# Kernel optimization log

Hardware: AMD Instinct MI355X
Metric: run time of the kernel (lower is better)

The kernel has to match this reference:

```python
import jax, jax.numpy as jnp
import numpy as np

N = 50000      # nodes
E = 1600000    # edges
D = 64         # in_channels (== hidden so layers stack)
H = 64         # hidden_channels
L = 3          # num_layers
G = 128        # graphs in batch
OUT = 1        # out_channels
BN_EPS = 1e-5


def setup_inputs() -> dict:
    key = jax.random.key(0)
    ks = jax.random.split(key, 8)
    s = 0.1
    x = jax.random.normal(ks[0], (N, D), dtype=jnp.float32)
    edge_index = jax.random.randint(ks[1], (2, E), 0, N, dtype=jnp.int64)
    batch = jnp.sort(jax.random.randint(ks[2], (N,), 0, G, dtype=jnp.int64))
    # stacked GINConv MLP params: Linear(D,H) -> BN(H) -> ReLU -> Linear(H,H)
    W1 = jax.random.normal(ks[3], (L, D, H), dtype=jnp.float32) * s
    b1 = jnp.zeros((L, H), jnp.float32)
    gamma = jnp.ones((L, H), jnp.float32)
    beta = jnp.zeros((L, H), jnp.float32)
    W2 = jax.random.normal(ks[4], (L, H, H), dtype=jnp.float32) * s
    b2 = jnp.zeros((L, H), jnp.float32)
    # head MLP: Linear(H,H) -> ReLU -> (dropout, eval mode) -> Linear(H,OUT)
    Wh1 = jax.random.normal(ks[5], (H, H), dtype=jnp.float32) * s
    bh1 = jnp.zeros((H,), jnp.float32)
    Wh2 = jax.random.normal(ks[6], (H, OUT), dtype=jnp.float32) * s
    bh2 = jnp.zeros((OUT,), jnp.float32)
    return dict(x=x, edge_index=edge_index, batch=batch,
                W1=W1, b1=b1, gamma=gamma, beta=beta, W2=W2, b2=b2,
                Wh1=Wh1, bh1=bh1, Wh2=Wh2, bh2=bh2)


def reference(x, edge_index, batch, W1, b1, gamma, beta, W2, b2, Wh1, bh1, Wh2, bh2):
    src, dst = edge_index[0], edge_index[1]

    def gin_layer(h, p):
        w1, bb1, g, be, w2, bb2 = p
        # scatter-add neighbor aggregation: sum_{j->i} h_j
        agg = jax.ops.segment_sum(h[src], dst, num_segments=N)  # [N, H]
        z = (agg + h) @ w1 + bb1  # (1+eps)*x + agg, eps=0; then Linear
        # BatchNorm1d (training-mode batch stats, biased var)
        mu = z.mean(0)
        var = ((z - mu) ** 2).mean(0)
        z = (z - mu) * jax.lax.rsqrt(var + BN_EPS) * g + be
        z = jax.nn.relu(z) @ w2 + bb2  # ReLU -> Linear (plain last layer)
        return jax.nn.relu(z), None    # outer .relu() in GIN.forward

    h, _ = jax.lax.scan(gin_layer, x, (W1, b1, gamma, beta, W2, b2))

    # global_mean_pool over batch ids
    cnt = jax.ops.segment_sum(jnp.ones((N, 1), h.dtype), batch, num_segments=G)
    pooled = jax.ops.segment_sum(h, batch, num_segments=G) / jnp.maximum(cnt, 1.0)

    # head MLP (dropout = identity in eval mode)
    return jax.nn.relu(pooled @ Wh1 + bh1) @ Wh2 + bh2
```

## Files before the change

kernel.cpp:

```cpp
#include <hip/hip_runtime.h>

#define N_NODES 50000
#define N_EDGES 1600000
#define HDIM 64
#define NLAYERS 3
#define NGRAPH 128
#define BN_EPS 1e-5f
#define CAP 96
#define NBINS 196
#define NBLK 782

__device__ __forceinline__ unsigned short f2bf(float f) {
    union { float f; unsigned u; } v; v.f = f;
    unsigned r = v.u + 0x7fffu + ((v.u >> 16) & 1u);
    return (unsigned short)(r >> 16);
}
__device__ __forceinline__ unsigned pack2(float a, float b) {
    return (unsigned)f2bf(a) | ((unsigned)f2bf(b) << 16);
}
__device__ __forceinline__ float bf2f(unsigned short b) {
    union { unsigned u; float f; } v; v.u = ((unsigned)b) << 16; return v.f;
}
__device__ __forceinline__ void acc8(float* a, uint4 v) {
    union { unsigned u; float f; } t;
    t.u = v.x << 16;         a[0] += t.f;
    t.u = v.x & 0xffff0000u; a[1] += t.f;
    t.u = v.y << 16;         a[2] += t.f;
    t.u = v.y & 0xffff0000u; a[3] += t.f;
    t.u = v.z << 16;         a[4] += t.f;
    t.u = v.z & 0xffff0000u; a[5] += t.f;
    t.u = v.w << 16;         a[6] += t.f;
    t.u = v.w & 0xffff0000u; a[7] += t.f;
}

__global__ __launch_bounds__(256) void hist1_kernel(
    const int* __restrict__ dst, int* __restrict__ gh)
{
    __shared__ int lh[NBINS];
    int tid = threadIdx.x;
    for (int i = tid; i < NBINS; i += 256) lh[i] = 0;
    __syncthreads();
    int t8 = blockIdx.x * 256 + tid;
    if (t8 < N_EDGES / 8) {
        int4 d0 = ((const int4*)dst)[t8 * 2];
        int4 d1 = ((const int4*)dst)[t8 * 2 + 1];
        atomicAdd(&lh[d0.x >> 8], 1);
        atomicAdd(&lh[d0.y >> 8], 1);
        atomicAdd(&lh[d0.z >> 8], 1);
        atomicAdd(&lh[d0.w >> 8], 1);
        atomicAdd(&lh[d1.x >> 8], 1);
        atomicAdd(&lh[d1.y >> 8], 1);
        atomicAdd(&lh[d1.z >> 8], 1);
        atomicAdd(&lh[d1.w >> 8], 1);
    }
    __syncthreads();
    for (int i = tid; i < NBINS; i += 256)
        gh[i * NBLK + blockIdx.x] = lh[i];
}

__global__ __launch_bounds__(256) void scan_bins_kernel(
    int* __restrict__ gh, int* __restrict__ binbase)
{
    __shared__ int wsum[4];
    __shared__ int woff[4];
    __shared__ int carry;
    int b = blockIdx.x;
    int tid = threadIdx.x, lane = tid & 63, wid = tid >> 6;
    if (tid == 0) carry = 0;
    __syncthreads();
    int* row = gh + b * NBLK;
    for (int base = 0; base < NBLK; base += 256) {
        int i = base + tid;
        int v = (i < NBLK) ? row[i] : 0;
        int incl = v;
        #pragma unroll
        for (int off = 1; off < 64; off <<= 1) {
            int t = __shfl_up(incl, off, 64);
            if (lane >= off) incl += t;
        }
        if (lane == 63) wsum[wid] = incl;
        __syncthreads();
        if (tid == 0) {
            int r = carry;
            #pragma unroll
            for (int w = 0; w < 4; ++w) { woff[w] = r; r += wsum[w]; }
            carry = r;
        }
        __syncthreads();
        if (i < NBLK) row[i] = woff[wid] + incl - v;
        __syncthreads();
    }
    if (tid == 0) binbase[b] = carry;
}

__global__ __launch_bounds__(256) void scan_base_kernel(int* __restrict__ binbase)
{
    __shared__ int wsum[4];
    __shared__ int woff[5];
    int tid = threadIdx.x, lane = tid & 63, wid = tid >> 6;
    int v = (tid < NBINS) ? binbase[tid] : 0;
    int incl = v;
    #pragma unroll
    for (int off = 1; off < 64; off <<= 1) {
        int t = __shfl_up(incl, off, 64);
        if (lane >= off) incl += t;
    }
    if (lane == 63) wsum[wid] = incl;
    __syncthreads();
    if (tid == 0) {
        int r = 0;
        #pragma unroll
        for (int w = 0; w < 4; ++w) { woff[w] = r; r += wsum[w]; }
        woff[4] = r;
    }
    __syncthreads();
    if (tid < NBINS) binbase[tid] = woff[wid] + incl - v;
    if (tid == 0) binbase[NBINS] = woff[4];
}

__global__ __launch_bounds__(256) void scatter_kernel(
    const int* __restrict__ src, const int* __restrict__ dst,
    const int* __restrict__ gh, const int* __restrict__ binbase,
    unsigned* __restrict__ packed)
{
    __shared__ int lbase[NBINS];
    int tid = threadIdx.x;
    for (int i = tid; i < NBINS; i += 256)
        lbase[i] = binbase[i] + gh[i * NBLK + blockIdx.x];
    __syncthreads();
    int t8 = blockIdx.x * 256 + tid;
    if (t8 >= N_EDGES / 8) return;
    int4 d0 = ((const int4*)dst)[t8 * 2];
    int4 d1 = ((const int4*)dst)[t8 * 2 + 1];
    int4 s0 = ((const int4*)src)[t8 * 2];
    int4 s1 = ((const int4*)src)[t8 * 2 + 1];
    int p0 = atomicAdd(&lbase[d0.x >> 8], 1);
    int p1 = atomicAdd(&lbase[d0.y >> 8], 1);
    int p2 = atomicAdd(&lbase[d0.z >> 8], 1);
    int p3 = atomicAdd(&lbase[d0.w >> 8], 1);
    int p4 = atomicAdd(&lbase[d1.x >> 8], 1);
    int p5 = atomicAdd(&lbase[d1.y >> 8], 1);
    int p6 = atomicAdd(&lbase[d1.z >> 8], 1);
    int p7 = atomicAdd(&lbase[d1.w >> 8], 1);
    packed[p0] = ((unsigned)d0.x << 16) | (unsigned)s0.x;
    packed[p1] = ((unsigned)d0.y << 16) | (unsigned)s0.y;
    packed[p2] = ((unsigned)d0.z << 16) | (unsigned)s0.z;
    packed[p3] = ((unsigned)d0.w << 16) | (unsigned)s0.w;
    packed[p4] = ((unsigned)d1.x << 16) | (unsigned)s1.x;
    packed[p5] = ((unsigned)d1.y << 16) | (unsigned)s1.y;
    packed[p6] = ((unsigned)d1.z << 16) | (unsigned)s1.z;
    packed[p7] = ((unsigned)d1.w << 16) | (unsigned)s1.w;
}

__global__ __launch_bounds__(256) void build_csr_kernel(
    const unsigned* __restrict__ packed, const int* __restrict__ binbase,
    unsigned short* __restrict__ col, int* __restrict__ cnt)
{
    __shared__ int lcnt[256];
    int b = blockIdx.x;
    int tid = threadIdx.x;
    lcnt[tid] = 0;
    __syncthreads();
    int e0 = binbase[b], e1 = binbase[b + 1];
    for (int e = e0 + tid; e < e1; e += 256) {
        unsigned p = packed[e];
        int d = (int)(p >> 16);
        int dl = d - (b << 8);
        int pos = atomicAdd(&lcnt[dl], 1);
        col[d * CAP + pos] = (unsigned short)(p & 0xffffu);
    }
    __syncthreads();
    int node = (b << 8) + tid;
    if (node < N_NODES) {
        int c = lcnt[tid];
        int end = (c + 7) & ~7;
        unsigned short* cp = col + node * CAP;
        for (int i = c; i < end; ++i) cp[i] = (unsigned short)N_NODES;
        cnt[node] = c;
    }
}

__global__ __launch_bounds__(256) void xcast_kernel(
    const float* __restrict__ x, unsigned short* __restrict__ xb)
{
    int t = blockIdx.x * 256 + threadIdx.x;
    if (t < 8)
        ((uint4*)(xb + (size_t)N_NODES * HDIM))[t] = make_uint4(0, 0, 0, 0);
    if (t >= N_NODES * HDIM / 8) return;
    float4 v0 = ((const float4*)x)[t * 2];
    float4 v1 = ((const float4*)x)[t * 2 + 1];
    uint4 o;
    o.x = pack2(v0.x, v0.y);
    o.y = pack2(v0.z, v0.w);
    o.z = pack2(v1.x, v1.y);
    o.w = pack2(v1.z, v1.w);
    ((uint4*)xb)[t] = o;
}

__global__ __launch_bounds__(256) void gather_gemm1_kernel(
    const unsigned short* __restrict__ hin, const int* __restrict__ cnt,
    const unsigned short* __restrict__ col, const float* __restrict__ W1,
    const float* __restrict__ b1, float* __restrict__ z,
    float* __restrict__ stats )
{
    __shared__ float sW[HDIM * HDIM];
    __shared__ float sIn[64][HDIM];
    __shared__ float sRedS[4][HDIM];
    __shared__ float sRedQ[4][HDIM];
    const uint4* hin4 = (const uint4*)hin;
    int tid = threadIdx.x;
    int w = tid >> 6, c = tid & 63;
    int sub = c >> 3;
    int q8 = c & 7;
    int row0 = blockIdx.x * 64;
    for (int i = tid; i < HDIM * HDIM; i += 256) sW[i] = W1[i];

    for (int rr = 0; rr < 16; ++rr) {
        int row = row0 + w * 16 + rr;
        if (row >= N_NODES) break;
        int nch = (cnt[row] + 7) >> 3;
        const unsigned short* cp = col + row * CAP + sub;
        float a[8] = {0.f, 0.f, 0.f, 0.f, 0.f, 0.f, 0.f, 0.f};
        int ch = 0;
        for (; ch + 4 <= nch; ch += 4) {
            int c0 = cp[ch * 8];
            int c1 = cp[ch * 8 + 8];
            int c2 = cp[ch * 8 + 16];
            int c3 = cp[ch * 8 + 24];
            uint4 v0 = hin4[c0 * 8 + q8];
            uint4 v1 = hin4[c1 * 8 + q8];
            uint4 v2 = hin4[c2 * 8 + q8];
            uint4 v3 = hin4[c3 * 8 + q8];
            acc8(a, v0); acc8(a, v1); acc8(a, v2); acc8(a, v3);
        }
        if (ch + 2 <= nch) {
            int c0 = cp[ch * 8];
            int c1 = cp[ch * 8 + 8];
            uint4 v0 = hin4[c0 * 8 + q8];
            uint4 v1 = hin4[c1 * 8 + q8];
            acc8(a, v0); acc8(a, v1);
            ch += 2;
        }
        if (ch < nch) {
            int c0 = cp[ch * 8];
            uint4 v0 = hin4[c0 * 8 + q8];
            acc8(a, v0);
        }
        #pragma unroll
        for (int off = 8; off < 64; off <<= 1) {
            #pragma unroll
            for (int j = 0; j < 8; ++j)
                a[j] += __shfl_xor(a[j], off, 64);
        }
        if (sub == 0) {
            uint4 sv = hin4[row * 8 + q8];
            acc8(a, sv);
            float4 o0, o1;
            o0.x = a[0]; o0.y = a[1]; o0.z = a[2]; o0.w = a[3];
            o1.x = a[4]; o1.y = a[5]; o1.z = a[6]; o1.w = a[7];
            *(float4*)&sIn[w * 16 + rr][q8 * 8] = o0;
            *(float4*)&sIn[w * 16 + rr][q8 * 8 + 4] = o1;
        }
    }
    float bias = b1[c];
    __syncthreads();

    float acc[16];
    #pragma unroll
    for (int r = 0; r < 16; ++r) acc[r] = bias;
    #pragma unroll 4
    for (int k4 = 0; k4 < HDIM; k4 += 4) {
        float w0 = sW[(k4 + 0) * HDIM + c];
        float w1 = sW[(k4 + 1) * HDIM + c];
        float w2 = sW[(k4 + 2) * HDIM + c];
        float w3 = sW[(k4 + 3) * HDIM + c];
        #pragma unroll
        for (int r = 0; r < 16; ++r) {
            float4 iv = *(const float4*)&sIn[w * 16 + r][k4];
            acc[r] = fmaf(iv.x, w0, acc[r]);
            acc[r] = fmaf(iv.y, w1, acc[r]);
            acc[r] = fmaf(iv.z, w2, acc[r]);
            acc[r] = fmaf(iv.w, w3, acc[r]);
        }
    }
    float s = 0.f, s2 = 0.f;
    #pragma unroll
    for (int r = 0; r < 16; ++r) {
        int row = row0 + w * 16 + r;
        if (row < N_NODES) {
            z[(size_t)row * HDIM + c] = acc[r];
            s += acc[r];
            s2 += acc[r] * acc[r];
        }
    }
    sRedS[w][c] = s;
    sRedQ[w][c] = s2;
    __syncthreads();
    if (tid < HDIM) {
        atomicAdd(&stats[c], sRedS[0][c] + sRedS[1][c] + sRedS[2][c] + sRedS[3][c]);
        atomicAdd(&stats[HDIM + c],
                  sRedQ[0][c] + sRedQ[1][c] + sRedQ[2][c] + sRedQ[3][c]);
    }
}

__global__ __launch_bounds__(256) void gemm2_kernel(
    const float* __restrict__ z, const float* __restrict__ W2,
    const float* __restrict__ b2, const float* __restrict__ stats,
    const float* __restrict__ gamma, const float* __restrict__ beta,
    unsigned short* __restrict__ hout)
{
    __shared__ float sW[HDIM * HDIM];
    __shared__ float sIn[64][HDIM];
    __shared__ float sSc[HDIM];
    __shared__ float sSh[HDIM];
    int tid = threadIdx.x;
    int w = tid >> 6, c = tid & 63;
    int row0 = blockIdx.x * 64;
    for (int i = tid; i < HDIM * HDIM; i += 256) sW[i] = W2[i];
    if (tid < HDIM) {
        float mu  = stats[tid] / (float)N_NODES;
        float var = stats[HDIM + tid] / (float)N_NODES - mu * mu;
        float sc  = gamma[tid] * rsqrtf(var + BN_EPS);
        sSc[tid] = sc;
        sSh[tid] = beta[tid] - mu * sc;
    }
    float bias = b2[c];
    __syncthreads();
    const float4* z4 = (const float4*)z;
    #pragma unroll
    for (int i = 0; i < 4; ++i) {
        int lin = tid + i * 256;
        int rr = lin >> 4, q = lin & 15;
        float4 v = (row0 + rr < N_NODES)
                       ? z4[(size_t)(row0 + rr) * 16 + q]
                       : make_float4(0.f, 0.f, 0.f, 0.f);
        int cb = q * 4;
        v.x = fmaxf(fmaf(v.x, sSc[cb + 0], sSh[cb + 0]), 0.f);
        v.y = fmaxf(fmaf(v.y, sSc[cb + 1], sSh[cb + 1]), 0.f);
        v.z = fmaxf(fmaf(v.z, sSc[cb + 2], sSh[cb + 2]), 0.f);
        v.w = fmaxf(fmaf(v.w, sSc[cb + 3], sSh[cb + 3]), 0.f);
        *(float4*)&sIn[rr][q * 4] = v;
    }
    __syncthreads();
    float acc[16];
    #pragma unroll
    for (int r = 0; r < 16; ++r) acc[r] = bias;
    #pragma unroll 4
    for (int k4 = 0; k4 < HDIM; k4 += 4) {
        float w0 = sW[(k4 + 0) * HDIM + c];
        float w1 = sW[(k4 + 1) * HDIM + c];
        float w2 = sW[(k4 + 2) * HDIM + c];
        float w3 = sW[(k4 + 3) * HDIM + c];
        #pragma unroll
        for (int r = 0; r < 16; ++r) {
            float4 iv = *(const float4*)&sIn[w * 16 + r][k4];
            acc[r] = fmaf(iv.x, w0, acc[r]);
            acc[r] = fmaf(iv.y, w1, acc[r]);
            acc[r] = fmaf(iv.z, w2, acc[r]);
            acc[r] = fmaf(iv.w, w3, acc[r]);
        }
    }
    #pragma unroll
    for (int r = 0; r < 16; ++r) {
        int row = row0 + w * 16 + r;
        if (row < N_NODES)
            hout[(size_t)row * HDIM + c] = f2bf(fmaxf(acc[r], 0.f));
    }
}

__global__ __launch_bounds__(256) void bounds_kernel(
    const int* __restrict__ batch, int* __restrict__ gstart,
    unsigned short* __restrict__ hA)
{
    int i = blockIdx.x * 256 + threadIdx.x;
    if (i < 8)
        ((uint4*)(hA + (size_t)N_NODES * HDIM))[i] = make_uint4(0, 0, 0, 0);
    if (i >= N_NODES) return;
    int g1 = batch[i];
    int g0 = (i == 0) ? -1 : batch[i - 1];
    for (int g = g0 + 1; g <= g1; ++g) gstart[g] = i;
    if (i == N_NODES - 1)
        for (int g = g1 + 1; g <= NGRAPH; ++g) gstart[g] = N_NODES;
}

__global__ __launch_bounds__(256) void pool_head_kernel(
    const unsigned short* __restrict__ h, const int* __restrict__ gstart,
    const float* __restrict__ Wh1, const float* __restrict__ bh1,
    const float* __restrict__ Wh2, const float* __restrict__ bh2,
    float* __restrict__ out)
{
    __shared__ float sW[HDIM * HDIM];
    __shared__ float sRed[4][HDIM];
    __shared__ float sMean[HDIM];
    int tid = threadIdx.x;
    int r = tid >> 6, c = tid & 63;
    int g = blockIdx.x;
    for (int i = tid; i < HDIM * HDIM; i += 256) sW[i] = Wh1[i];
    int s0 = gstart[g], s1 = gstart[g + 1];
    float acc = 0.f;
    for (int row = s0 + r; row < s1; row += 4)
        acc += bf2f(h[(size_t)row * HDIM + c]);
    sRed[r][c] = acc;
    __syncthreads();
    if (r == 0) {
        float cntf = (float)(s1 - s0);
        sMean[c] = (sRed[0][c] + sRed[1][c] + sRed[2][c] + sRed[3][c]) /
                   fmaxf(cntf, 1.0f);
    }
    __syncthreads();
    if (r == 0) {
        float a = bh1[c];
        #pragma unroll
        for (int k = 0; k < HDIM; ++k)
            a = fmaf(sMean[k], sW[k * HDIM + c], a);
        a = fmaxf(a, 0.f);
        float p = a * Wh2[c];
        #pragma unroll
        for (int off = 32; off > 0; off >>= 1)
            p += __shfl_down(p, off, 64);
        if (c == 0) out[g] = p + bh2[0];
    }
}

extern "C" void kernel_launch(void* const* d_in, const int* in_sizes, int n_in,
                              void* d_out, int out_size, void* d_ws, size_t ws_size,
                              hipStream_t stream)
{
    const float* x     = (const float*)d_in[0];
    const int*   ei    = (const int*)d_in[1];
    const int*   batch = (const int*)d_in[2];
    const float* W1    = (const float*)d_in[3];
    const float* b1    = (const float*)d_in[4];
    const float* gamma = (const float*)d_in[5];
    const float* beta  = (const float*)d_in[6];
    const float* W2    = (const float*)d_in[7];
    const float* b2    = (const float*)d_in[8];
    const float* Wh1   = (const float*)d_in[9];
    const float* bh1   = (const float*)d_in[10];
    const float* Wh2   = (const float*)d_in[11];
    const float* bh2   = (const float*)d_in[12];
    float* out = (float*)d_out;

    float*          ws  = (float*)d_ws;
    float*          hB  = ws;
    unsigned short* hA  = (unsigned short*)(hB + (size_t)N_NODES * HDIM);
    unsigned short* xb  = hA + (size_t)(N_NODES + 1) * HDIM;
    int*   gstart  = (int*)(xb + (size_t)(N_NODES + 1) * HDIM + 32);
    int*   cnt     = gstart + NGRAPH + 1;
    float* stats   = (float*)(cnt + N_NODES);
    unsigned short* col = (unsigned short*)(stats + 3 * 2 * HDIM);
    unsigned* packed = (unsigned*)(col + (size_t)N_NODES * CAP);
    int*   gh      = (int*)(packed + N_EDGES);
    int*   binbase = gh + NBINS * NBLK;

    const int* src = ei;
    const int* dst = ei + N_EDGES;

    int gemmGrid = (N_NODES + 63) / 64;
    int nodeGrid = (N_NODES + 255) / 256;
    int castGrid = (N_NODES * HDIM / 8 + 255) / 256;

    hipMemsetAsync(stats, 0, 3 * 2 * HDIM * sizeof(float), stream);
    hist1_kernel<<<NBLK, 256, 0, stream>>>(dst, gh);
    scan_bins_kernel<<<NBINS, 256, 0, stream>>>(gh, binbase);
    scan_base_kernel<<<1, 256, 0, stream>>>(binbase);
    scatter_kernel<<<NBLK, 256, 0, stream>>>(src, dst, gh, binbase, packed);
    build_csr_kernel<<<NBINS, 256, 0, stream>>>(packed, binbase, col, cnt);
    xcast_kernel<<<castGrid, 256, 0, stream>>>(x, xb);
    bounds_kernel<<<nodeGrid, 256, 0, stream>>>(batch, gstart, hA);

    for (int l = 0; l < NLAYERS; ++l) {
        const unsigned short* hin = (l == 0) ? xb : hA;
        float* statsl = stats + l * 2 * HDIM;
        gather_gemm1_kernel<<<gemmGrid, 256, 0, stream>>>(
            hin, cnt, col, W1 + l * HDIM * HDIM, b1 + l * HDIM, hB, statsl);
        gemm2_kernel<<<gemmGrid, 256, 0, stream>>>(
            hB, W2 + l * HDIM * HDIM, b2 + l * HDIM, statsl,
            gamma + l * HDIM, beta + l * HDIM, hA);
    }

    pool_head_kernel<<<NGRAPH, 256, 0, stream>>>(hA, gstart, Wh1, bh1, Wh2, bh2, out);
}
```

Baseline: 350.6 us.

## Shrink gather-GEMM1 blocks to 16 rows and replace stat atomics with two-stage reduction

The fused gather+GEMM1 kernel now handles 16 rows per block (3125 blocks) instead of 64, and each wave does a per-row dot product against a transposed, padded W1 in shared memory right after gathering that row. The aim is more parallelism and better latency hiding for the irregular gather. BatchNorm statistics are now written as per-block partials and reduced by two small kernels instead of global atomics, which also removes the memset. The cost is two extra launches per layer, a W1 load into shared memory for every one of the many small blocks, and per-row GEMM work that no longer reuses each weight load across several rows.

```diff
diff --git a/kernel.cpp b/kernel.cpp
--- a/kernel.cpp
+++ b/kernel.cpp
@@ -9,6 +9,8 @@
 #define CAP 96
 #define NBINS 196
 #define NBLK 782
+#define FUSEGRID 3125
+#define GEMMGRID 782
 
 __device__ __forceinline__ unsigned short f2bf(float f) {
     union { float f; unsigned u; } v; v.f = f;
@@ -201,10 +203,10 @@
     const unsigned short* __restrict__ hin, const int* __restrict__ cnt,
     const unsigned short* __restrict__ col, const float* __restrict__ W1,
     const float* __restrict__ b1, float* __restrict__ z,
-    float* __restrict__ stats )
-{
-    __shared__ float sW[HDIM * HDIM];
-    __shared__ float sIn[64][HDIM];
+    float* __restrict__ partials )
+{
+    __shared__ float sWT[HDIM * 68];
+    __shared__ float sRow[4][HDIM];
     __shared__ float sRedS[4][HDIM];
     __shared__ float sRedQ[4][HDIM];
     const uint4* hin4 = (const uint4*)hin;
@@ -212,12 +214,16 @@
     int w = tid >> 6, c = tid & 63;
     int sub = c >> 3;
     int q8 = c & 7;
-    int row0 = blockIdx.x * 64;
-    for (int i = tid; i < HDIM * HDIM; i += 256) sW[i] = W1[i];
-
-    for (int rr = 0; rr < 16; ++rr) {
-        int row = row0 + w * 16 + rr;
-        if (row >= N_NODES) break;
+    for (int i = tid; i < HDIM * HDIM; i += 256) {
+        int k = i >> 6, cc = i & 63;
+        sWT[cc * 68 + k] = W1[i];
+    }
+    float bias = b1[c];
+    float s = 0.f, s2 = 0.f;
+    __syncthreads();
+    int row0 = blockIdx.x * 16 + w * 4;
+    for (int rr = 0; rr < 4; ++rr) {
+        int row = row0 + rr;
         int nch = (cnt[row] + 7) >> 3;
         const unsigned short* cp = col + row * CAP + sub;
         float a[8] = {0.f, 0.f, 0.f, 0.f, 0.f, 0.f, 0.f, 0.f};
@@ -252,61 +258,77 @@
             for (int j = 0; j < 8; ++j)
                 a[j] += __shfl_xor(a[j], off, 64);
         }
+        acc8(a, hin4[row * 8 + q8]);
         if (sub == 0) {
-            uint4 sv = hin4[row * 8 + q8];
-            acc8(a, sv);
             float4 o0, o1;
             o0.x = a[0]; o0.y = a[1]; o0.z = a[2]; o0.w = a[3];
             o1.x = a[4]; o1.y = a[5]; o1.z = a[6]; o1.w = a[7];
-            *(float4*)&sIn[w * 16 + rr][q8 * 8] = o0;
-            *(float4*)&sIn[w * 16 + rr][q8 * 8 + 4] = o1;
-        }
-    }
-    float bias = b1[c];
-    __syncthreads();
-
-    float acc[16];
-    #pragma unroll
-    for (int r = 0; r < 16; ++r) acc[r] = bias;
-    #pragma unroll 4
-    for (int k4 = 0; k4 < HDIM; k4 += 4) {
-        float w0 = sW[(k4 + 0) * HDIM + c];
-        float w1 = sW[(k4 + 1) * HDIM + c];
-        float w2 = sW[(k4 + 2) * HDIM + c];
-        float w3 = sW[(k4 + 3) * HDIM + c];
-        #pragma unroll
-        for (int r = 0; r < 16; ++r) {
-            float4 iv = *(const float4*)&sIn[w * 16 + r][k4];
-            acc[r] = fmaf(iv.x, w0, acc[r]);
-            acc[r] = fmaf(iv.y, w1, acc[r]);
-            acc[r] = fmaf(iv.z, w2, acc[r]);
-            acc[r] = fmaf(iv.w, w3, acc[r]);
-        }
-    }
-    float s = 0.f, s2 = 0.f;
-    #pragma unroll
-    for (int r = 0; r < 16; ++r) {
-        int row = row0 + w * 16 + r;
-        if (row < N_NODES) {
-            z[(size_t)row * HDIM + c] = acc[r];
-            s += acc[r];
-            s2 += acc[r] * acc[r];
-        }
+            *(float4*)&sRow[w][q8 * 8] = o0;
+            *(float4*)&sRow[w][q8 * 8 + 4] = o1;
+        }
+        __builtin_amdgcn_wave_barrier();
+        float ac0 = 0.f, ac1 = 0.f, ac2 = 0.f, ac3 = 0.f;
+        #pragma unroll
+        for (int k4 = 0; k4 < 16; ++k4) {
+            float4 rv = *(const float4*)&sRow[w][k4 * 4];
+            float4 wv = *(const float4*)&sWT[c * 68 + k4 * 4];
+            ac0 = fmaf(rv.x, wv.x, ac0);
+            ac1 = fmaf(rv.y, wv.y, ac1);
+            ac2 = fmaf(rv.z, wv.z, ac2);
+            ac3 = fmaf(rv.w, wv.w, ac3);
+        }
+        float zv = bias + (ac0 + ac1) + (ac2 + ac3);
+        z[(size_t)row * HDIM + c] = zv;
+        s += zv;
+        s2 += zv * zv;
+        __builtin_amdgcn_wave_barrier();
     }
     sRedS[w][c] = s;
     sRedQ[w][c] = s2;
     __syncthreads();
+    if (tid < 128) {
+        int chn = tid & 63;
+        float v = (tid < 64)
+            ? sRedS[0][chn] + sRedS[1][chn] + sRedS[2][chn] + sRedS[3][chn]
+            : sRedQ[0][chn] + sRedQ[1][chn] + sRedQ[2][chn] + sRedQ[3][chn];
+        partials[blockIdx.x * 128 + tid] = v;
+    }
+}
+
+__global__ __launch_bounds__(128) void stats_red1_kernel(
+    const float* __restrict__ partials, float* __restrict__ part2)
+{
+    int c = threadIdx.x;
+    int slice = blockIdx.x;
+    float acc = 0.f;
+    for (int i = slice; i < FUSEGRID; i += 64)
+        acc += partials[i * 128 + c];
+    part2[slice * 128 + c] = acc;
+}
+
+__global__ __launch_bounds__(128) void stats_red2_kernel(
+    const float* __restrict__ part2, const float* __restrict__ gamma,
+    const float* __restrict__ beta, float* __restrict__ scsh)
+{
+    __shared__ float tot[128];
+    int tid = threadIdx.x;
+    float acc = 0.f;
+    for (int s = 0; s < 64; ++s)
+        acc += part2[s * 128 + tid];
+    tot[tid] = acc;
+    __syncthreads();
     if (tid < HDIM) {
-        atomicAdd(&stats[c], sRedS[0][c] + sRedS[1][c] + sRedS[2][c] + sRedS[3][c]);
-        atomicAdd(&stats[HDIM + c],
-                  sRedQ[0][c] + sRedQ[1][c] + sRedQ[2][c] + sRedQ[3][c]);
+        float mu  = tot[tid] / (float)N_NODES;
+        float var = tot[HDIM + tid] / (float)N_NODES - mu * mu;
+        float sc  = gamma[tid] * rsqrtf(var + BN_EPS);
+        scsh[tid] = sc;
+        scsh[HDIM + tid] = beta[tid] - mu * sc;
     }
 }
 
 __global__ __launch_bounds__(256) void gemm2_kernel(
     const float* __restrict__ z, const float* __restrict__ W2,
-    const float* __restrict__ b2, const float* __restrict__ stats,
-    const float* __restrict__ gamma, const float* __restrict__ beta,
+    const float* __restrict__ b2, const float* __restrict__ scsh,
     unsigned short* __restrict__ hout)
 {
     __shared__ float sW[HDIM * HDIM];
@@ -318,11 +340,8 @@
     int row0 = blockIdx.x * 64;
     for (int i = tid; i < HDIM * HDIM; i += 256) sW[i] = W2[i];
     if (tid < HDIM) {
-        float mu  = stats[tid] / (float)N_NODES;
-        float var = stats[HDIM + tid] / (float)N_NODES - mu * mu;
-        float sc  = gamma[tid] * rsqrtf(var + BN_EPS);
-        sSc[tid] = sc;
-        sSh[tid] = beta[tid] - mu * sc;
+        sSc[tid] = scsh[tid];
+        sSh[tid] = scsh[HDIM + tid];
     }
     float bias = b2[c];
     __syncthreads();
@@ -447,8 +466,10 @@
     unsigned short* xb  = hA + (size_t)(N_NODES + 1) * HDIM;
     int*   gstart  = (int*)(xb + (size_t)(N_NODES + 1) * HDIM + 32);
     int*   cnt     = gstart + NGRAPH + 1;
-    float* stats   = (float*)(cnt + N_NODES);
-    unsigned short* col = (unsigned short*)(stats + 3 * 2 * HDIM);
+    float* scsh    = (float*)(cnt + N_NODES);
+    float* partials = scsh + 2 * HDIM;
+    float* part2   = partials + (size_t)FUSEGRID * 128;
+    unsigned short* col = (unsigned short*)(part2 + 64 * 128);
     unsigned* packed = (unsigned*)(col + (size_t)N_NODES * CAP);
     int*   gh      = (int*)(packed + N_EDGES);
     int*   binbase = gh + NBINS * NBLK;
@@ -456,11 +477,9 @@
     const int* src = ei;
     const int* dst = ei + N_EDGES;
 
-    int gemmGrid = (N_NODES + 63) / 64;
     int nodeGrid = (N_NODES + 255) / 256;
     int castGrid = (N_NODES * HDIM / 8 + 255) / 256;
 
-    hipMemsetAsync(stats, 0, 3 * 2 * HDIM * sizeof(float), stream);
     hist1_kernel<<<NBLK, 256, 0, stream>>>(dst, gh);
     scan_bins_kernel<<<NBINS, 256, 0, stream>>>(gh, binbase);
     scan_base_kernel<<<1, 256, 0, stream>>>(binbase);
@@ -471,12 +490,13 @@
 
     for (int l = 0; l < NLAYERS; ++l) {
         const unsigned short* hin = (l == 0) ? xb : hA;
-        float* statsl = stats + l * 2 * HDIM;
-        gather_gemm1_kernel<<<gemmGrid, 256, 0, stream>>>(
-            hin, cnt, col, W1 + l * HDIM * HDIM, b1 + l * HDIM, hB, statsl);
-        gemm2_kernel<<<gemmGrid, 256, 0, stream>>>(
-            hB, W2 + l * HDIM * HDIM, b2 + l * HDIM, statsl,
-            gamma + l * HDIM, beta + l * HDIM, hA);
+        gather_gemm1_kernel<<<FUSEGRID, 256, 0, stream>>>(
+            hin, cnt, col, W1 + l * HDIM * HDIM, b1 + l * HDIM, hB, partials);
+        stats_red1_kernel<<<64, 128, 0, stream>>>(partials, part2);
+        stats_red2_kernel<<<1, 128, 0, stream>>>(
+            part2, gamma + l * HDIM, beta + l * HDIM, scsh);
+        gemm2_kernel<<<GEMMGRID, 256, 0, stream>>>(
+            hB, W2 + l * HDIM * HDIM, b2 + l * HDIM, scsh, hA);
     }
 
     pool_head_kernel<<<NGRAPH, 256, 0, stream>>>(hA, gstart, Wh1, bh1, Wh2, bh2, out);
```

New measurement: 314.9 us. 1.11x faster.
